# Kernel tuning notes

Measured on AMD Instinct MI355X. Metric: run time of the kernel, lower is better.

Reference implementation:

```python
import jax, jax.numpy as jnp
import numpy as np

EPS = 1e-6

def poincare_pairwise_distance(x, c):
    """x: (B,N,E) points in Poincare ball, c: (C,E) centroids. Returns (B,N,C)."""
    x2 = jnp.sum(x * x, axis=-1)                  # (B,N)
    c2 = jnp.sum(c * c, axis=-1)                  # (C,)
    xc = jnp.einsum('bne,ce->bnc', x, c)          # (B,N,C)
    sq = jnp.maximum(x2[..., None] + c2[None, None, :] - 2.0 * xc, 0.0)  # ||x-c||^2
    den = (1.0 - x2)[..., None] * (1.0 - c2)[None, None, :]
    arg = 1.0 + 2.0 * sq / jnp.maximum(den, EPS)
    return jnp.arccosh(jnp.maximum(arg, 1.0 + EPS))

def setup_inputs() -> dict:
    key = jax.random.key(0)
    k1, k2 = jax.random.split(key)
    B, N, E, C = 32, 4096, 64, 256
    # scale so points lie strictly inside the unit ball (valid hyperbolic coords)
    node_repr = jax.random.normal(k1, (B, N, E), dtype=jnp.float32) * 0.05
    mask = jnp.ones((B, N, 1), dtype=jnp.float32)
    centroid = jax.random.normal(k2, (C, E), dtype=jnp.float32) * 0.01
    return {"node_repr": node_repr, "mask": mask, "centroid": centroid}

def reference(node_repr, mask, centroid):
    dist = poincare_pairwise_distance(node_repr, centroid)   # (B,N,C)
    dist = dist * mask                                       # mask: (B,N,1) broadcasts
    graph_dist = jnp.sum(dist, axis=1) / jnp.sum(mask, axis=1)  # (B,C)
    return graph_dist, dist
```

## Files before the change

kernel.cpp:

```cpp
#include <hip/hip_runtime.h>
#include <math.h>

#define E_DIM 64
#define C_DIM 256
#define CKP   72
#define EPS_F 1e-6f

typedef __attribute__((ext_vector_type(8))) short short8;
typedef __attribute__((ext_vector_type(4))) float f32x4;

__device__ __forceinline__ unsigned short f2bf(float f) {
    unsigned int u = __float_as_uint(f);
    u += 0x7FFFu + ((u >> 16) & 1u);
    return (unsigned short)(u >> 16);
}

__global__ __launch_bounds__(256) void cdist_mfma(
    const float* __restrict__ x,
    const float* __restrict__ mask,
    const float* __restrict__ cent,
    float*       __restrict__ graph_acc,
    float*       __restrict__ dist,
    int N)
{
    const int tid  = threadIdx.x;
    const int w    = tid >> 6;
    const int lane = tid & 63;
    const int l15  = lane & 15;
    const int q    = lane >> 4;
    const int n0   = blockIdx.x * 64;
    const int b    = blockIdx.y;

    __shared__ __align__(16) unsigned short sA[64 * CKP];
    __shared__ __align__(16) unsigned short sB[C_DIM * CKP];
    __shared__ float s_a[64], s_rb[64], s_k[64];
    __shared__ float s_c2[C_DIM], s_rd2[C_DIM];

    const float* xblk = x + ((size_t)b * N + n0) * E_DIM;

    #pragma unroll
    for (int it = 0; it < 4; ++it) {
        const int flat = it * 1024 + tid * 4;
        float4 v = *reinterpret_cast<const float4*>(xblk + flat);
        const int r = flat >> 6, e = flat & 63;
        ushort4 h;
        h.x = f2bf(v.x); h.y = f2bf(v.y); h.z = f2bf(v.z); h.w = f2bf(v.w);
        *reinterpret_cast<ushort4*>(&sA[r * CKP + e]) = h;
    }
    #pragma unroll
    for (int it = 0; it < 16; ++it) {
        const int flat = it * 1024 + tid * 4;
        float4 v = *reinterpret_cast<const float4*>(cent + flat);
        const int r = flat >> 6, e = flat & 63;
        ushort4 h;
        h.x = f2bf(v.x); h.y = f2bf(v.y); h.z = f2bf(v.z); h.w = f2bf(v.w);
        *reinterpret_cast<ushort4*>(&sB[r * CKP + e]) = h;
    }
    if (tid < 64) {
        const float* xr = xblk + tid * E_DIM;
        float s = 0.f;
        #pragma unroll
        for (int e = 0; e < E_DIM; e += 4) {
            float4 v = *reinterpret_cast<const float4*>(xr + e);
            s = fmaf(v.x, v.x, s); s = fmaf(v.y, v.y, s);
            s = fmaf(v.z, v.z, s); s = fmaf(v.w, v.w, s);
        }
        s_a [tid] = s;
        s_rb[tid] = __builtin_amdgcn_rcpf(1.f - s);
        s_k [tid] = 0.69314718056f * mask[(size_t)b * N + n0 + tid];
    }
    {
        const float* cr = cent + tid * E_DIM;
        float s = 0.f;
        #pragma unroll
        for (int e = 0; e < E_DIM; e += 4) {
            float4 v = *reinterpret_cast<const float4*>(cr + e);
            s = fmaf(v.x, v.x, s); s = fmaf(v.y, v.y, s);
            s = fmaf(v.z, v.z, s); s = fmaf(v.w, v.w, s);
        }
        s_c2 [tid] = s;
        s_rd2[tid] = 2.f * __builtin_amdgcn_rcpf(1.f - s);
    }
    __syncthreads();

    short8 bfrag[4][2];
    #pragma unroll
    for (int ct = 0; ct < 4; ++ct) {
        const int c = w * 64 + ct * 16 + l15;
        #pragma unroll
        for (int kf = 0; kf < 2; ++kf)
            bfrag[ct][kf] = *reinterpret_cast<const short8*>(&sB[c * CKP + kf * 32 + q * 8]);
    }
    float c2v[4], rd2v[4], gsum[4];
    #pragma unroll
    for (int ct = 0; ct < 4; ++ct) {
        const int c = w * 64 + ct * 16 + l15;
        c2v[ct] = s_c2[c]; rd2v[ct] = s_rd2[c]; gsum[ct] = 0.f;
    }

    const size_t rowbase = (size_t)b * N + n0;

    #pragma unroll
    for (int rt = 0; rt < 4; ++rt) {
        const int r0 = rt * 16;
        short8 a0 = *reinterpret_cast<const short8*>(&sA[(r0 + l15) * CKP + q * 8]);
        short8 a1 = *reinterpret_cast<const short8*>(&sA[(r0 + l15) * CKP + 32 + q * 8]);

        f32x4 acc[4];
        #pragma unroll
        for (int ct = 0; ct < 4; ++ct) {
            f32x4 z = {0.f, 0.f, 0.f, 0.f};
            z = __builtin_amdgcn_mfma_f32_16x16x32_bf16(a0, bfrag[ct][0], z, 0, 0, 0);
            z = __builtin_amdgcn_mfma_f32_16x16x32_bf16(a1, bfrag[ct][1], z, 0, 0, 0);
            acc[ct] = z;
        }

        float ar[4], rbr[4], kr[4];
        #pragma unroll
        for (int reg = 0; reg < 4; ++reg) {
            const int rr = r0 + q * 4 + reg;
            ar[reg] = s_a[rr]; rbr[reg] = s_rb[rr]; kr[reg] = s_k[rr];
        }
        #pragma unroll
        for (int ct = 0; ct < 4; ++ct) {
            const int c = w * 64 + ct * 16 + l15;
            #pragma unroll
            for (int reg = 0; reg < 4; ++reg) {
                const float dot = acc[ct][reg];
                float sq = fmaf(-2.f, dot, ar[reg] + c2v[ct]);
                sq = fmaxf(sq, 0.f);
                float u = fmaxf(sq * (rbr[reg] * rd2v[ct]), EPS_F);
                float t = u + __builtin_amdgcn_sqrtf(fmaf(u, u, u + u));
                const float d = __builtin_amdgcn_logf(1.f + t) * kr[reg];
                dist[(rowbase + r0 + q * 4 + reg) * C_DIM + c] = d;
                gsum[ct] += d;
            }
        }
    }

    #pragma unroll
    for (int ct = 0; ct < 4; ++ct) {
        float s = gsum[ct];
        s += __shfl_xor(s, 16);
        s += __shfl_xor(s, 32);
        if (q == 0)
            atomicAdd(&graph_acc[b * C_DIM + w * 64 + ct * 16 + l15], s);
    }
}

__global__ __launch_bounds__(C_DIM) void cdist_finalize(
    const float* __restrict__ mask,
    float*       __restrict__ graph,
    int N)
{
    const int b = blockIdx.x;
    const int t = threadIdx.x;

    float s = 0.f;
    for (int n = t; n < N; n += C_DIM) s += mask[(size_t)b * N + n];
    #pragma unroll
    for (int off = 32; off > 0; off >>= 1) s += __shfl_down(s, off, 64);

    __shared__ float partial[4];
    __shared__ float total_s;
    if ((t & 63) == 0) partial[t >> 6] = s;
    __syncthreads();
    if (t == 0) total_s = partial[0] + partial[1] + partial[2] + partial[3];
    __syncthreads();

    graph[b * C_DIM + t] /= total_s;
}

extern "C" void kernel_launch(void* const* d_in, const int* in_sizes, int n_in,
                              void* d_out, int out_size, void* d_ws, size_t ws_size,
                              hipStream_t stream) {
    const float* x    = (const float*)d_in[0];
    const float* mask = (const float*)d_in[1];
    const float* cent = (const float*)d_in[2];
    float* out = (float*)d_out;

    const long long BN = in_sizes[1];
    const int E = in_sizes[0] / (int)BN;
    const int C = in_sizes[2] / E;
    const int B = (int)(((long long)out_size - BN * C) / C);
    const int N = (int)(BN / B);

    float* graph_acc = out;
    float* dist_out  = out + (size_t)B * C;

    hipMemsetAsync(graph_acc, 0, (size_t)B * C * sizeof(float), stream);

    dim3 grid(N / 64, B);
    cdist_mfma<<<grid, 256, 0, stream>>>(x, mask, cent, graph_acc, dist_out, N);
    cdist_finalize<<<dim3(B), C_DIM, 0, stream>>>(mask, graph_acc, N);
}
```

Baseline: 191.9 us.

## Precompute centroid MFMA fragments once and load x directly into registers

Result: no change. 191.4 us (-0.2%).

```diff
diff --git a/kernel.cpp b/kernel.cpp
--- a/kernel.cpp
+++ b/kernel.cpp
@@ -3,8 +3,8 @@
 
 #define E_DIM 64
 #define C_DIM 256
-#define CKP   72
 #define EPS_F 1e-6f
+#define LN2_F 0.69314718056f
 
 typedef __attribute__((ext_vector_type(8))) short short8;
 typedef __attribute__((ext_vector_type(4))) float f32x4;
@@ -15,10 +15,74 @@
     return (unsigned short)(u >> 16);
 }
 
+__device__ __forceinline__ short8 pack8(float4 a, float4 b) {
+    short8 h;
+    h[0] = (short)f2bf(a.x); h[1] = (short)f2bf(a.y);
+    h[2] = (short)f2bf(a.z); h[3] = (short)f2bf(a.w);
+    h[4] = (short)f2bf(b.x); h[5] = (short)f2bf(b.y);
+    h[6] = (short)f2bf(b.z); h[7] = (short)f2bf(b.w);
+    return h;
+}
+
+#define WS_F    0
+#define WS_C2   32768
+#define WS_RD2  33792
+#define WS_INVM 34816
+
+__global__ __launch_bounds__(C_DIM) void cdist_pre(
+    const float* __restrict__ cent,
+    const float* __restrict__ mask,
+    unsigned char* __restrict__ ws,
+    int N)
+{
+    const int t = threadIdx.x;
+    if (blockIdx.x == 0) {
+        float r[E_DIM];
+        const float* cr = cent + t * E_DIM;
+        #pragma unroll
+        for (int e = 0; e < E_DIM; e += 4) {
+            float4 v = *reinterpret_cast<const float4*>(cr + e);
+            r[e] = v.x; r[e+1] = v.y; r[e+2] = v.z; r[e+3] = v.w;
+        }
+        float c2 = 0.f;
+        #pragma unroll
+        for (int e = 0; e < E_DIM; ++e) c2 = fmaf(r[e], r[e], c2);
+        ((float*)(ws + WS_C2))[t]  = c2;
+        ((float*)(ws + WS_RD2))[t] = 2.f / (1.f - c2);
+
+        const int ct16 = t >> 4, l15 = t & 15;
+        short8* F = (short8*)(ws + WS_F);
+        #pragma unroll
+        for (int kf = 0; kf < 2; ++kf) {
+            #pragma unroll
+            for (int q = 0; q < 4; ++q) {
+                short8 h;
+                #pragma unroll
+                for (int j = 0; j < 8; ++j)
+                    h[j] = (short)f2bf(r[kf * 32 + q * 8 + j]);
+                F[(ct16 * 2 + kf) * 64 + 16 * q + l15] = h;
+            }
+        }
+    } else {
+        const int b = blockIdx.x - 1;
+        float s = 0.f;
+        for (int n = t; n < N; n += C_DIM) s += mask[(size_t)b * N + n];
+        #pragma unroll
+        for (int off = 32; off > 0; off >>= 1) s += __shfl_down(s, off, 64);
+        __shared__ float partial[4];
+        if ((t & 63) == 0) partial[t >> 6] = s;
+        __syncthreads();
+        if (t == 0) {
+            float tot = partial[0] + partial[1] + partial[2] + partial[3];
+            ((float*)(ws + WS_INVM))[b] = 1.f / tot;
+        }
+    }
+}
+
 __global__ __launch_bounds__(256) void cdist_mfma(
     const float* __restrict__ x,
     const float* __restrict__ mask,
-    const float* __restrict__ cent,
+    const unsigned char* __restrict__ ws,
     float*       __restrict__ graph_acc,
     float*       __restrict__ dist,
     int N)
@@ -31,80 +95,52 @@
     const int n0   = blockIdx.x * 64;
     const int b    = blockIdx.y;
 
-    __shared__ __align__(16) unsigned short sA[64 * CKP];
-    __shared__ __align__(16) unsigned short sB[C_DIM * CKP];
-    __shared__ float s_a[64], s_rb[64], s_k[64];
-    __shared__ float s_c2[C_DIM], s_rd2[C_DIM];
-
-    const float* xblk = x + ((size_t)b * N + n0) * E_DIM;
-
-    #pragma unroll
-    for (int it = 0; it < 4; ++it) {
-        const int flat = it * 1024 + tid * 4;
-        float4 v = *reinterpret_cast<const float4*>(xblk + flat);
-        const int r = flat >> 6, e = flat & 63;
-        ushort4 h;
-        h.x = f2bf(v.x); h.y = f2bf(v.y); h.z = f2bf(v.z); h.w = f2bf(v.w);
-        *reinterpret_cast<ushort4*>(&sA[r * CKP + e]) = h;
-    }
-    #pragma unroll
-    for (int it = 0; it < 16; ++it) {
-        const int flat = it * 1024 + tid * 4;
-        float4 v = *reinterpret_cast<const float4*>(cent + flat);
-        const int r = flat >> 6, e = flat & 63;
-        ushort4 h;
-        h.x = f2bf(v.x); h.y = f2bf(v.y); h.z = f2bf(v.z); h.w = f2bf(v.w);
-        *reinterpret_cast<ushort4*>(&sB[r * CKP + e]) = h;
-    }
-    if (tid < 64) {
-        const float* xr = xblk + tid * E_DIM;
-        float s = 0.f;
-        #pragma unroll
-        for (int e = 0; e < E_DIM; e += 4) {
-            float4 v = *reinterpret_cast<const float4*>(xr + e);
-            s = fmaf(v.x, v.x, s); s = fmaf(v.y, v.y, s);
-            s = fmaf(v.z, v.z, s); s = fmaf(v.w, v.w, s);
-        }
-        s_a [tid] = s;
-        s_rb[tid] = __builtin_amdgcn_rcpf(1.f - s);
-        s_k [tid] = 0.69314718056f * mask[(size_t)b * N + n0 + tid];
-    }
-    {
-        const float* cr = cent + tid * E_DIM;
-        float s = 0.f;
-        #pragma unroll
-        for (int e = 0; e < E_DIM; e += 4) {
-            float4 v = *reinterpret_cast<const float4*>(cr + e);
-            s = fmaf(v.x, v.x, s); s = fmaf(v.y, v.y, s);
-            s = fmaf(v.z, v.z, s); s = fmaf(v.w, v.w, s);
-        }
-        s_c2 [tid] = s;
-        s_rd2[tid] = 2.f * __builtin_amdgcn_rcpf(1.f - s);
-    }
-    __syncthreads();
+    const short8* F   = (const short8*)(ws + WS_F);
+    const float*  c2w = (const float*)(ws + WS_C2);
+    const float*  rd2w= (const float*)(ws + WS_RD2);
 
     short8 bfrag[4][2];
+    #pragma unroll
+    for (int ct = 0; ct < 4; ++ct)
+        #pragma unroll
+        for (int kf = 0; kf < 2; ++kf)
+            bfrag[ct][kf] = F[((w * 4 + ct) * 2 + kf) * 64 + lane];
+
+    float c2v[4], rd2v[4], gsum[4];
     #pragma unroll
     for (int ct = 0; ct < 4; ++ct) {
         const int c = w * 64 + ct * 16 + l15;
-        #pragma unroll
-        for (int kf = 0; kf < 2; ++kf)
-            bfrag[ct][kf] = *reinterpret_cast<const short8*>(&sB[c * CKP + kf * 32 + q * 8]);
-    }
-    float c2v[4], rd2v[4], gsum[4];
-    #pragma unroll
-    for (int ct = 0; ct < 4; ++ct) {
-        const int c = w * 64 + ct * 16 + l15;
-        c2v[ct] = s_c2[c]; rd2v[ct] = s_rd2[c]; gsum[ct] = 0.f;
+        c2v[ct] = c2w[c]; rd2v[ct] = rd2w[c]; gsum[ct] = 0.f;
     }
 
     const size_t rowbase = (size_t)b * N + n0;
 
     #pragma unroll
     for (int rt = 0; rt < 4; ++rt) {
-        const int r0 = rt * 16;
-        short8 a0 = *reinterpret_cast<const short8*>(&sA[(r0 + l15) * CKP + q * 8]);
-        short8 a1 = *reinterpret_cast<const short8*>(&sA[(r0 + l15) * CKP + 32 + q * 8]);
+        const size_t row = rowbase + rt * 16 + l15;
+        const float* xr = x + row * E_DIM + q * 8;
+        float4 v0 = *reinterpret_cast<const float4*>(xr);
+        float4 v1 = *reinterpret_cast<const float4*>(xr + 4);
+        float4 v2 = *reinterpret_cast<const float4*>(xr + 32);
+        float4 v3 = *reinterpret_cast<const float4*>(xr + 36);
+
+        float ss = 0.f;
+        ss = fmaf(v0.x, v0.x, ss); ss = fmaf(v0.y, v0.y, ss);
+        ss = fmaf(v0.z, v0.z, ss); ss = fmaf(v0.w, v0.w, ss);
+        ss = fmaf(v1.x, v1.x, ss); ss = fmaf(v1.y, v1.y, ss);
+        ss = fmaf(v1.z, v1.z, ss); ss = fmaf(v1.w, v1.w, ss);
+        ss = fmaf(v2.x, v2.x, ss); ss = fmaf(v2.y, v2.y, ss);
+        ss = fmaf(v2.z, v2.z, ss); ss = fmaf(v2.w, v2.w, ss);
+        ss = fmaf(v3.x, v3.x, ss); ss = fmaf(v3.y, v3.y, ss);
+        ss = fmaf(v3.z, v3.z, ss); ss = fmaf(v3.w, v3.w, ss);
+        ss += __shfl_xor(ss, 16);
+        ss += __shfl_xor(ss, 32);
+
+        const float rbrow = __builtin_amdgcn_rcpf(1.f - ss);
+        const float krow  = LN2_F * mask[row];
+
+        short8 a0 = pack8(v0, v1);
+        short8 a1 = pack8(v2, v3);
 
         f32x4 acc[4];
         #pragma unroll
@@ -118,8 +154,10 @@
         float ar[4], rbr[4], kr[4];
         #pragma unroll
         for (int reg = 0; reg < 4; ++reg) {
-            const int rr = r0 + q * 4 + reg;
-            ar[reg] = s_a[rr]; rbr[reg] = s_rb[rr]; kr[reg] = s_k[rr];
+            const int src = q * 4 + reg;
+            ar[reg]  = __shfl(ss,    src);
+            rbr[reg] = __shfl(rbrow, src);
+            kr[reg]  = __shfl(krow,  src);
         }
         #pragma unroll
         for (int ct = 0; ct < 4; ++ct) {
@@ -132,43 +170,21 @@
                 float u = fmaxf(sq * (rbr[reg] * rd2v[ct]), EPS_F);
                 float t = u + __builtin_amdgcn_sqrtf(fmaf(u, u, u + u));
                 const float d = __builtin_amdgcn_logf(1.f + t) * kr[reg];
-                dist[(rowbase + r0 + q * 4 + reg) * C_DIM + c] = d;
+                dist[(rowbase + rt * 16 + q * 4 + reg) * C_DIM + c] = d;
                 gsum[ct] += d;
             }
         }
     }
 
+    const float inv = ((const float*)(ws + WS_INVM))[b];
     #pragma unroll
     for (int ct = 0; ct < 4; ++ct) {
         float s = gsum[ct];
         s += __shfl_xor(s, 16);
         s += __shfl_xor(s, 32);
         if (q == 0)
-            atomicAdd(&graph_acc[b * C_DIM + w * 64 + ct * 16 + l15], s);
-    }
-}
-
-__global__ __launch_bounds__(C_DIM) void cdist_finalize(
-    const float* __restrict__ mask,
-    float*       __restrict__ graph,
-    int N)
-{
-    const int b = blockIdx.x;
-    const int t = threadIdx.x;
-
-    float s = 0.f;
-    for (int n = t; n < N; n += C_DIM) s += mask[(size_t)b * N + n];
-    #pragma unroll
-    for (int off = 32; off > 0; off >>= 1) s += __shfl_down(s, off, 64);
-
-    __shared__ float partial[4];
-    __shared__ float total_s;
-    if ((t & 63) == 0) partial[t >> 6] = s;
-    __syncthreads();
-    if (t == 0) total_s = partial[0] + partial[1] + partial[2] + partial[3];
-    __syncthreads();
-
-    graph[b * C_DIM + t] /= total_s;
+            atomicAdd(&graph_acc[b * C_DIM + w * 64 + ct * 16 + l15], s * inv);
+    }
 }
 
 extern "C" void kernel_launch(void* const* d_in, const int* in_sizes, int n_in,
@@ -187,10 +203,10 @@
 
     float* graph_acc = out;
     float* dist_out  = out + (size_t)B * C;
+    unsigned char* ws = (unsigned char*)d_ws;
 
     hipMemsetAsync(graph_acc, 0, (size_t)B * C * sizeof(float), stream);
 
-    dim3 grid(N / 64, B);
-    cdist_mfma<<<grid, 256, 0, stream>>>(x, mask, cent, graph_acc, dist_out, N);
-    cdist_finalize<<<dim3(B), C_DIM, 0, stream>>>(mask, graph_acc, N);
-}
+    cdist_pre<<<dim3(B + 1), C_DIM, 0, stream>>>(cent, mask, ws, N);
+    cdist_mfma<<<dim3(N / 64, B), 256, 0, stream>>>(x, mask, ws, graph_acc, dist_out, N);
+}
```
